# Performance work log

Measured on AMD Instinct MI355X. Metric: run time of the kernel, lower is better.

The kernel has to match this reference:

```python
import jax, jax.numpy as jnp
import numpy as np

EMBED_DIM = 1024
NUM_HEADS = 16
HEAD_DIM = EMBED_DIM // NUM_HEADS
SCALE = HEAD_DIM ** -0.5


def setup_inputs() -> dict:
    key = jax.random.key(0)
    ks = jax.random.split(key, 9)
    B, S, D = 32, 577, EMBED_DIM
    std = 1.0 / np.sqrt(D)
    inp = {
        "hidden_states": jax.random.normal(ks[0], (B, S, D), dtype=jnp.float32),
        "q_w": jax.random.normal(ks[1], (D, D), dtype=jnp.float32) * std,
        "q_b": jax.random.normal(ks[2], (D,), dtype=jnp.float32) * 0.01,
        "k_w": jax.random.normal(ks[3], (D, D), dtype=jnp.float32) * std,
        "k_b": jax.random.normal(ks[4], (D,), dtype=jnp.float32) * 0.01,
        "v_w": jax.random.normal(ks[5], (D, D), dtype=jnp.float32) * std,
        "v_b": jax.random.normal(ks[6], (D,), dtype=jnp.float32) * 0.01,
        "o_w": jax.random.normal(ks[7], (D, D), dtype=jnp.float32) * std,
        "o_b": jax.random.normal(ks[8], (D,), dtype=jnp.float32) * 0.01,
    }
    return inp


def reference(hidden_states, q_w, q_b, k_w, k_b, v_w, v_b, o_w, o_b):
    B, S, D = hidden_states.shape
    H, Dh = NUM_HEADS, HEAD_DIM

    def proj(w, b):
        # torch Linear: x @ w.T + b ; reshape to [B, H, S, Dh]
        y = jnp.einsum('bsd,ed->bse', hidden_states, w) + b
        return y.reshape(B, S, H, Dh).transpose(0, 2, 1, 3)

    q = proj(q_w, q_b)
    k = proj(k_w, k_b)
    v = proj(v_w, v_b)

    scores = jnp.einsum('bhqd,bhkd->bhqk', q * SCALE, k)  # [B,H,S,S]
    attn = jax.nn.softmax(scores, axis=-1)
    out = jnp.einsum('bhqk,bhkd->bhqd', attn, v)  # [B,H,S,Dh]
    out = out.transpose(0, 2, 1, 3).reshape(B, S, D)
    return jnp.einsum('bsd,ed->bse', out, o_w) + o_b
```

## Files before the change

### kernel.cpp

```cpp
#include <hip/hip_runtime.h>
#include <hip/hip_bf16.h>
#include <stdint.h>

#define B_   32
#define S_   577
#define SP   640
#define D_   1024
#define H_   16
#define DH   64
#define BH_  (B_*H_)
#define M_   (B_*S_)
#define MP2  18688
#define SCALE_ 0.125f
#define LOG2E_ 1.44269504088896f

typedef __bf16 bf16;
typedef __bf16 bf16x8 __attribute__((ext_vector_type(8)));
typedef __bf16 bf16x4 __attribute__((ext_vector_type(4)));
typedef float  f32x4  __attribute__((ext_vector_type(4)));

__device__ __forceinline__ void gload16(const bf16* g, bf16* l) {
    __builtin_amdgcn_global_load_lds((__attribute__((address_space(1))) void*)g,
                                     (__attribute__((address_space(3))) void*)l, 16, 0, 0);
}

__global__ void cast_kernel(const float* __restrict__ in, bf16* __restrict__ out, int n4) {
    int i = blockIdx.x * blockDim.x + threadIdx.x;
    if (i >= n4) return;
    float4 v = ((const float4*)in)[i];
    bf16x4 o;
    o[0] = (bf16)v.x; o[1] = (bf16)v.y; o[2] = (bf16)v.z; o[3] = (bf16)v.w;
    ((bf16x4*)out)[i] = o;
}

__global__ void cast4_kernel(const float* __restrict__ w0, const float* __restrict__ w1,
                             const float* __restrict__ w2, const float* __restrict__ w3,
                             bf16* __restrict__ o0, bf16* __restrict__ o1,
                             bf16* __restrict__ o2, bf16* __restrict__ o3) {
    int i = blockIdx.x * blockDim.x + threadIdx.x;
    int seg = i >> 18, r = i & 262143;
    const float* in = (seg == 0) ? w0 : (seg == 1) ? w1 : (seg == 2) ? w2 : w3;
    bf16* out       = (seg == 0) ? o0 : (seg == 1) ? o1 : (seg == 2) ? o2 : o3;
    float4 v = ((const float4*)in)[r];
    bf16x4 o;
    o[0] = (bf16)v.x; o[1] = (bf16)v.y; o[2] = (bf16)v.z; o[3] = (bf16)v.w;
    ((bf16x4*)out)[r] = o;
}

__device__ __forceinline__ void stage256(const bf16* __restrict__ A, const bf16* __restrict__ B,
                                         int m0, int n0, int K, int kt, bf16* SMbuf) {
    const int tid = threadIdx.x;
    const int wave = tid >> 6;
    #pragma unroll
    for (int ld = 0; ld < 8; ++ld) {
        int li  = ld * 512 + tid;
        int row = (li >> 3) & 255;
        int ch  = (li & 7) ^ (row & 7);
        const bf16* g = ((ld < 4) ? (A + (size_t)(m0 + row) * K)
                                  : (B + (size_t)(n0 + row) * K)) + kt * 64 + ch * 8;
        bf16* l = SMbuf + (size_t)(ld * 512 + wave * 64) * 8;
        gload16(g, l);
    }
}

__device__ __forceinline__ void compute256(const bf16* SMbuf, f32x4 acc[8][4],
                                           int wm, int wn, int r16, int c4) {
    #pragma unroll
    for (int kk = 0; kk < 2; ++kk) {
        bf16x8 bq[4];
        #pragma unroll
        for (int j = 0; j < 4; ++j) {
            int row = wn * 64 + j * 16 + r16;
            int c   = (kk * 4 + c4) ^ (row & 7);
            bq[j] = *(const bf16x8*)(SMbuf + 16384 + row * 64 + c * 8);
        }
        #pragma unroll
        for (int i = 0; i < 8; ++i) {
            int row = wm * 128 + i * 16 + r16;
            int c   = (kk * 4 + c4) ^ (row & 7);
            bf16x8 a = *(const bf16x8*)(SMbuf + row * 64 + c * 8);
            #pragma unroll
            for (int j = 0; j < 4; ++j)
                acc[i][j] = __builtin_amdgcn_mfma_f32_16x16x32_bf16(a, bq[j], acc[i][j], 0, 0, 0);
        }
    }
}

__global__ __launch_bounds__(512, 2) void gemm_qkv(const bf16* __restrict__ A, const bf16* __restrict__ Bw,
                                                   const float* __restrict__ qb, const float* __restrict__ kb,
                                                   const float* __restrict__ vb,
                                                   bf16* __restrict__ qk, bf16* __restrict__ vT) {
    __shared__ __align__(16) bf16 SM[2 * 32768];
    const int bx = blockIdx.x;
    const int bm = bx / 12, bn = bx % 12;
    const int m0 = bm * 256, n0 = bn * 256;
    const int tid = threadIdx.x;
    const int lane = tid & 63, wave = tid >> 6;
    const int wm = wave >> 2, wn = wave & 3;
    const int r16 = lane & 15, c4 = lane >> 4;

    f32x4 acc[8][4];
    #pragma unroll
    for (int i = 0; i < 8; ++i)
        #pragma unroll
        for (int j = 0; j < 4; ++j)
            #pragma unroll
            for (int r = 0; r < 4; ++r) acc[i][j][r] = 0.0f;

    stage256(A, Bw, m0, n0, 1024, 0, SM);
    __syncthreads();
    for (int kt = 0; kt < 16; ++kt) {
        if (kt < 15) stage256(A, Bw, m0, n0, 1024, kt + 1, SM + ((kt + 1) & 1) * 32768);
        compute256(SM + (kt & 1) * 32768, acc, wm, wn, r16, c4);
        __syncthreads();
    }

    if (bn < 8) {
        const float* barr = (bn < 4) ? qb : kb;
        const float mul = (bn < 4) ? SCALE_ * LOG2E_ : 1.0f;
        #pragma unroll
        for (int j = 0; j < 4; ++j) {
            int n = n0 + wn * 64 + j * 16 + r16;
            float bias = barr[n & 1023];
            #pragma unroll
            for (int i = 0; i < 8; ++i) {
                #pragma unroll
                for (int r = 0; r < 4; ++r) {
                    int m = m0 + wm * 128 + i * 16 + c4 * 4 + r;
                    if (m < M_) qk[(size_t)m * 2048 + n] = (bf16)((acc[i][j][r] + bias) * mul);
                }
            }
        }
    } else {
        const int bnp = bn - 8;
        bf16* Ts = SM;
        #pragma unroll
        for (int mh = 0; mh < 2; ++mh) {
            if (wm == mh) {
                #pragma unroll
                for (int j = 0; j < 4; ++j) {
                    int nl = wn * 64 + j * 16 + r16;
                    float bias = vb[bnp * 256 + nl];
                    #pragma unroll
                    for (int i = 0; i < 8; ++i) {
                        #pragma unroll
                        for (int r = 0; r < 4; ++r) {
                            int tr = i * 16 + c4 * 4 + r;
                            Ts[tr * 259 + nl] = (bf16)(acc[i][j][r] + bias);
                        }
                    }
                }
            }
            __syncthreads();
            {
                int ml = tid & 127, nh = tid >> 7;
                int gm = m0 + mh * 128 + ml;
                if (gm < M_) {
                    unsigned bb = (unsigned)gm / 577u, s = (unsigned)gm - bb * 577u;
                    bf16* dst = vT + ((size_t)((bb * 16 + bnp * 4 + nh) * 64)) * SP + s;
                    const bf16* src = Ts + ml * 259 + nh * 64;
                    #pragma unroll 8
                    for (int j = 0; j < 64; ++j) dst[(size_t)j * SP] = src[j];
                }
            }
            __syncthreads();
        }
    }
}

__device__ __forceinline__ void stage_out(const bf16* __restrict__ A, const bf16* __restrict__ B,
                                          int m0, int n0, int kt, bf16* SMbuf) {
    const int tid = threadIdx.x;
    const int wave = tid >> 6;
    #pragma unroll
    for (int ld = 0; ld < 2; ++ld) {
        int li  = ld * 512 + tid;
        int row = li >> 3;
        int ch  = (li & 7) ^ (row & 7);
        gload16(A + (size_t)(m0 + row) * 1024 + kt * 64 + ch * 8,
                SMbuf + (size_t)(ld * 512 + wave * 64) * 8);
    }
    #pragma unroll
    for (int ld = 0; ld < 4; ++ld) {
        int li  = ld * 512 + tid;
        int row = li >> 3;
        int ch  = (li & 7) ^ (row & 7);
        gload16(B + (size_t)(n0 + row) * 1024 + kt * 64 + ch * 8,
                SMbuf + 8192 + (size_t)(ld * 512 + wave * 64) * 8);
    }
}

__global__ __launch_bounds__(512, 2) void gemm_out(const bf16* __restrict__ A, const bf16* __restrict__ Bw,
                                                   const float* __restrict__ ob, float* __restrict__ out) {
    __shared__ __align__(16) bf16 SM[2 * 24576];
    const int bx = blockIdx.x;
    const int bm = bx >> 2, bn = bx & 3;
    const int m0 = bm * 128, n0 = bn * 256;
    const int tid = threadIdx.x;
    const int lane = tid & 63, wave = tid >> 6;
    const int wm = wave >> 2, wn = wave & 3;
    const int r16 = lane & 15, c4 = lane >> 4;

    f32x4 acc[4][4];
    #pragma unroll
    for (int i = 0; i < 4; ++i)
        #pragma unroll
        for (int j = 0; j < 4; ++j)
            #pragma unroll
            for (int r = 0; r < 4; ++r) acc[i][j][r] = 0.0f;

    stage_out(A, Bw, m0, n0, 0, SM);
    __syncthreads();
    for (int kt = 0; kt < 16; ++kt) {
        if (kt < 15) stage_out(A, Bw, m0, n0, kt + 1, SM + ((kt + 1) & 1) * 24576);
        const bf16* SMbuf = SM + (kt & 1) * 24576;
        #pragma unroll
        for (int kk = 0; kk < 2; ++kk) {
            bf16x8 bq[4];
            #pragma unroll
            for (int j = 0; j < 4; ++j) {
                int row = wn * 64 + j * 16 + r16;
                int c   = (kk * 4 + c4) ^ (row & 7);
                bq[j] = *(const bf16x8*)(SMbuf + 8192 + row * 64 + c * 8);
            }
            #pragma unroll
            for (int i = 0; i < 4; ++i) {
                int row = wm * 64 + i * 16 + r16;
                int c   = (kk * 4 + c4) ^ (row & 7);
                bf16x8 a = *(const bf16x8*)(SMbuf + row * 64 + c * 8);
                #pragma unroll
                for (int j = 0; j < 4; ++j)
                    acc[i][j] = __builtin_amdgcn_mfma_f32_16x16x32_bf16(a, bq[j], acc[i][j], 0, 0, 0);
            }
        }
        __syncthreads();
    }

    #pragma unroll
    for (int j = 0; j < 4; ++j) {
        int n = n0 + wn * 64 + j * 16 + r16;
        float bias = ob[n];
        #pragma unroll
        for (int i = 0; i < 4; ++i) {
            #pragma unroll
            for (int r = 0; r < 4; ++r) {
                int m = m0 + wm * 64 + i * 16 + c4 * 4 + r;
                if (m < M_) out[(size_t)m * 1024 + n] = acc[i][j][r] + bias;
            }
        }
    }
}

__global__ __launch_bounds__(256) void attn_kernel(const bf16* __restrict__ qk,
                                                   const bf16* __restrict__ vT, bf16* __restrict__ obuf) {
    __shared__ __align__(16) bf16 KV[2][2][4096];
    __shared__ __align__(16) char Pls[4 * 2048];
    const int orig = blockIdx.x;
    const int xcd = orig & 7;
    const int t   = orig >> 3;
    const int qt  = t % 5, bhg = t / 5;
    const int bh  = bhg * 8 + xcd;
    const int b   = bh >> 4, h = bh & 15;
    const int tid = threadIdx.x;
    const int lane = tid & 63, wave = tid >> 6;
    const int r16 = lane & 15, c4 = lane >> 4;
    const int q0  = qt * 128 + wave * 32;
    const int swz = (r16 & 7) << 4;

    const bf16* qp = qk + (size_t)(b * 577) * 2048 + h * 64;
    const bf16* kp = qp + 1024;
    const bf16* vp = vT + (size_t)bh * 64 * SP;

    bf16x8 aq[2][2];
    #pragma unroll
    for (int qf = 0; qf < 2; ++qf)
        #pragma unroll
        for (int c = 0; c < 2; ++c)
            aq[qf][c] = *(const bf16x8*)(qp + (size_t)(q0 + qf * 16 + r16) * 2048 + c * 32 + c4 * 8);

    float mi[2] = {-3.0e38f, -3.0e38f};
    float li[2] = {0.0f, 0.0f};
    f32x4 accO[2][4];
    #pragma unroll
    for (int qf = 0; qf < 2; ++qf)
        #pragma unroll
        for (int nt = 0; nt < 4; ++nt)
            #pragma unroll
            for (int r = 0; r < 4; ++r) accO[qf][nt][r] = 0.0f;

    char* pbase = Pls + wave * 2048 + r16 * 128;

    auto stageKV = [&](int kt, int buf) {
        #pragma unroll
        for (int half = 0; half < 2; ++half) {
            int li  = half * 256 + tid;
            int row = li >> 3;
            int ch  = (li & 7) ^ (row & 7);
            bf16* lk = &KV[buf][0][(size_t)(half * 256 + wave * 64) * 8];
            bf16* lv = &KV[buf][1][(size_t)(half * 256 + wave * 64) * 8];
            gload16(kp + (size_t)(kt * 64 + row) * 2048 + ch * 8, lk);
            gload16(vp + (size_t)row * SP + kt * 64 + ch * 8, lv);
        }
    };

    stageKV(0, 0);
    __syncthreads();

    for (int kt = 0; kt < 10; ++kt) {
        const int buf = kt & 1;
        if (kt < 9) stageKV(kt + 1, buf ^ 1);

        bf16x8 kf[4][2];
        #pragma unroll
        for (int nt = 0; nt < 4; ++nt)
            #pragma unroll
            for (int c = 0; c < 2; ++c) {
                int row = nt * 16 + r16;
                int cc  = (c * 4 + c4) ^ (row & 7);
                kf[nt][c] = *(const bf16x8*)(&KV[buf][0][row * 64 + cc * 8]);
            }
        f32x4 sc[2][4];
        #pragma unroll
        for (int qf = 0; qf < 2; ++qf)
            #pragma unroll
            for (int nt = 0; nt < 4; ++nt) {
                f32x4 z = {0.0f, 0.0f, 0.0f, 0.0f};
                z = __builtin_amdgcn_mfma_f32_16x16x32_bf16(kf[nt][0], aq[qf][0], z, 0, 0, 0);
                sc[qf][nt] = __builtin_amdgcn_mfma_f32_16x16x32_bf16(kf[nt][1], aq[qf][1], z, 0, 0, 0);
            }

        bf16x8 vf[4][2];
        #pragma unroll
        for (int ntd = 0; ntd < 4; ++ntd)
            #pragma unroll
            for (int kk = 0; kk < 2; ++kk) {
                int row = ntd * 16 + r16;
                int cc  = (kk * 4 + c4) ^ (row & 7);
                vf[ntd][kk] = *(const bf16x8*)(&KV[buf][1][row * 64 + cc * 8]);
            }

        #pragma unroll
        for (int qf = 0; qf < 2; ++qf) {
            if (kt == 9) {
                #pragma unroll
                for (int nt = 0; nt < 4; ++nt)
                    #pragma unroll
                    for (int r = 0; r < 4; ++r)
                        if (576 + nt * 16 + c4 * 4 + r >= S_) sc[qf][nt][r] = -3.0e38f;
            }
            float pmax = sc[qf][0][0];
            #pragma unroll
            for (int nt = 0; nt < 4; ++nt)
                #pragma unroll
                for (int r = 0; r < 4; ++r) pmax = fmaxf(pmax, sc[qf][nt][r]);
            pmax = fmaxf(pmax, __shfl_xor(pmax, 16));
            pmax = fmaxf(pmax, __shfl_xor(pmax, 32));

            const bool vrow = (q0 + qf * 16 + r16) < S_;
            int ok = (!vrow) || (pmax <= mi[qf] + 8.0f);
            if (!__all(ok)) {
                float mnew = fmaxf(mi[qf], pmax);
                float fsc  = __builtin_amdgcn_exp2f(mi[qf] - mnew);
                mi[qf] = mnew;
                li[qf] *= fsc;
                float fs0 = __shfl(fsc, c4 * 4 + 0);
                float fs1 = __shfl(fsc, c4 * 4 + 1);
                float fs2 = __shfl(fsc, c4 * 4 + 2);
                float fs3 = __shfl(fsc, c4 * 4 + 3);
                #pragma unroll
                for (int nt = 0; nt < 4; ++nt) {
                    accO[qf][nt][0] *= fs0; accO[qf][nt][1] *= fs1;
                    accO[qf][nt][2] *= fs2; accO[qf][nt][3] *= fs3;
                }
            }
            float p[4][4];
            float rs = 0.0f;
            #pragma unroll
            for (int nt = 0; nt < 4; ++nt)
                #pragma unroll
                for (int r = 0; r < 4; ++r) {
                    p[nt][r] = __builtin_amdgcn_exp2f(sc[qf][nt][r] - mi[qf]);
                    rs += p[nt][r];
                }
            rs += __shfl_xor(rs, 16);
            rs += __shfl_xor(rs, 32);
            li[qf] += rs;
            #pragma unroll
            for (int nt = 0; nt < 4; ++nt) {
                bf16x4 pk;
                pk[0] = (bf16)p[nt][0]; pk[1] = (bf16)p[nt][1];
                pk[2] = (bf16)p[nt][2]; pk[3] = (bf16)p[nt][3];
                *(bf16x4*)(pbase + ((nt * 32 + c4 * 8) ^ swz)) = pk;
            }

            bf16x8 pf[2];
            #pragma unroll
            for (int kk = 0; kk < 2; ++kk)
                pf[kk] = *(const bf16x8*)(pbase + ((kk * 64 + c4 * 16) ^ swz));
            #pragma unroll
            for (int ntd = 0; ntd < 4; ++ntd)
                #pragma unroll
                for (int kk = 0; kk < 2; ++kk)
                    accO[qf][ntd] = __builtin_amdgcn_mfma_f32_16x16x32_bf16(pf[kk], vf[ntd][kk], accO[qf][ntd], 0, 0, 0);
        }

        __syncthreads();
    }

    #pragma unroll
    for (int qf = 0; qf < 2; ++qf) {
        float inv = 1.0f / li[qf];
        float rl0 = __shfl(inv, c4 * 4 + 0);
        float rl1 = __shfl(inv, c4 * 4 + 1);
        float rl2 = __shfl(inv, c4 * 4 + 2);
        float rl3 = __shfl(inv, c4 * 4 + 3);
        #pragma unroll
        for (int ntd = 0; ntd < 4; ++ntd) {
            #pragma unroll
            for (int r = 0; r < 4; ++r) {
                int s = q0 + qf * 16 + c4 * 4 + r;
                if (s < S_) {
                    float rl = (r == 0) ? rl0 : (r == 1) ? rl1 : (r == 2) ? rl2 : rl3;
                    obuf[((size_t)(b * S_ + s)) * 1024 + h * 64 + ntd * 16 + r16] =
                        (bf16)(accO[qf][ntd][r] * rl);
                }
            }
        }
    }
}

extern "C" void kernel_launch(void* const* d_in, const int* in_sizes, int n_in,
                              void* d_out, int out_size, void* d_ws, size_t ws_size,
                              hipStream_t stream) {
    const float* hs = (const float*)d_in[0];
    const float* qw = (const float*)d_in[1];
    const float* qb = (const float*)d_in[2];
    const float* kw = (const float*)d_in[3];
    const float* kb = (const float*)d_in[4];
    const float* vw = (const float*)d_in[5];
    const float* vb = (const float*)d_in[6];
    const float* ow = (const float*)d_in[7];
    const float* ob = (const float*)d_in[8];

    char* ws = (char*)d_ws;
    size_t off = 0;
    auto alloc = [&](size_t bytes) { void* p = ws + off; off += (bytes + 255) & ~255UL; return p; };
    bf16* hsA  = (bf16*)alloc((size_t)MP2 * 1024 * 2);
    bf16* wqkv = (bf16*)alloc((size_t)3072 * 1024 * 2);
    bf16* wo   = (bf16*)alloc((size_t)1024 * 1024 * 2);
    bf16* qk   = (bf16*)alloc((size_t)MP2 * 2048 * 2);
    bf16* vT   = (bf16*)alloc((size_t)BH_ * 64 * SP * 2);

    hipMemsetAsync(vT, 0, (size_t)BH_ * 64 * SP * 2, stream);

    int n4h = M_ * 1024 / 4;
    cast_kernel<<<(n4h + 255) / 256, 256, 0, stream>>>(hs, hsA, n4h);
    cast4_kernel<<<4096, 256, 0, stream>>>(qw, kw, vw, ow,
                                           wqkv, wqkv + 1048576, wqkv + 2097152, wo);

    gemm_qkv<<<73 * 12, 512, 0, stream>>>(hsA, wqkv, qb, kb, vb, qk, vT);
    attn_kernel<<<2560, 256, 0, stream>>>(qk, vT, hsA);
    gemm_out<<<145 * 4, 512, 0, stream>>>(hsA, wo, ob, (float*)d_out);
}
```

Baseline: 369.2 us.

## Enlarge attention query tile, fuse cast kernels, zero only V padding

The attention kernel now gives each block 256 query rows (64 per wave, four 16-row fragments) across 3 query tiles instead of 128 rows across 5, so each K/V tile staged in LDS is reused by more queries. Fragments lying entirely past the sequence end are skipped. The two fp32-to-bf16 cast kernels are merged into one launch, and the full-buffer memset of vT is replaced by a small kernel that zeros only the padded tail columns. The larger query tile raises register pressure and can lower occupancy, and fewer blocks are launched, which may balance worse across CUs.

```diff
diff --git a/kernel.cpp b/kernel.cpp
--- a/kernel.cpp
+++ b/kernel.cpp
@@ -24,27 +24,33 @@
                                      (__attribute__((address_space(3))) void*)l, 16, 0, 0);
 }
 
-__global__ void cast_kernel(const float* __restrict__ in, bf16* __restrict__ out, int n4) {
+__global__ void cast_all(const float* __restrict__ hs, const float* __restrict__ qw,
+                         const float* __restrict__ kw, const float* __restrict__ vw,
+                         const float* __restrict__ ow,
+                         bf16* __restrict__ hsA, bf16* __restrict__ wq, bf16* __restrict__ wk,
+                         bf16* __restrict__ wv, bf16* __restrict__ wo) {
+    const int N4H = M_ * 256;
     int i = blockIdx.x * blockDim.x + threadIdx.x;
-    if (i >= n4) return;
-    float4 v = ((const float4*)in)[i];
-    bf16x4 o;
-    o[0] = (bf16)v.x; o[1] = (bf16)v.y; o[2] = (bf16)v.z; o[3] = (bf16)v.w;
-    ((bf16x4*)out)[i] = o;
-}
-
-__global__ void cast4_kernel(const float* __restrict__ w0, const float* __restrict__ w1,
-                             const float* __restrict__ w2, const float* __restrict__ w3,
-                             bf16* __restrict__ o0, bf16* __restrict__ o1,
-                             bf16* __restrict__ o2, bf16* __restrict__ o3) {
-    int i = blockIdx.x * blockDim.x + threadIdx.x;
-    int seg = i >> 18, r = i & 262143;
-    const float* in = (seg == 0) ? w0 : (seg == 1) ? w1 : (seg == 2) ? w2 : w3;
-    bf16* out       = (seg == 0) ? o0 : (seg == 1) ? o1 : (seg == 2) ? o2 : o3;
+    if (i >= N4H + 4 * 262144) return;
+    const float* in; bf16* out; int r;
+    if (i < N4H) { in = hs; out = hsA; r = i; }
+    else {
+        int j = i - N4H, seg = j >> 18; r = j & 262143;
+        in  = (seg == 0) ? qw : (seg == 1) ? kw : (seg == 2) ? vw : ow;
+        out = (seg == 0) ? wq : (seg == 1) ? wk : (seg == 2) ? wv : wo;
+    }
     float4 v = ((const float4*)in)[r];
     bf16x4 o;
     o[0] = (bf16)v.x; o[1] = (bf16)v.y; o[2] = (bf16)v.z; o[3] = (bf16)v.w;
     ((bf16x4*)out)[r] = o;
+}
+
+__global__ void zero_vpad(bf16* __restrict__ vT) {
+    int i = blockIdx.x * blockDim.x + threadIdx.x;
+    if (i >= BH_ * 64) return;
+    bf16* row = vT + (size_t)i * SP + S_;
+    #pragma unroll
+    for (int j = 0; j < SP - S_; ++j) row[j] = (bf16)0.0f;
 }
 
 __device__ __forceinline__ void stage256(const bf16* __restrict__ A, const bf16* __restrict__ B,
@@ -258,31 +264,31 @@
     const int orig = blockIdx.x;
     const int xcd = orig & 7;
     const int t   = orig >> 3;
-    const int qt  = t % 5, bhg = t / 5;
+    const int qt  = t % 3, bhg = t / 3;
     const int bh  = bhg * 8 + xcd;
     const int b   = bh >> 4, h = bh & 15;
     const int tid = threadIdx.x;
     const int lane = tid & 63, wave = tid >> 6;
     const int r16 = lane & 15, c4 = lane >> 4;
-    const int q0  = qt * 128 + wave * 32;
+    const int q0  = qt * 256 + wave * 64;
     const int swz = (r16 & 7) << 4;
 
     const bf16* qp = qk + (size_t)(b * 577) * 2048 + h * 64;
     const bf16* kp = qp + 1024;
     const bf16* vp = vT + (size_t)bh * 64 * SP;
 
-    bf16x8 aq[2][2];
-    #pragma unroll
-    for (int qf = 0; qf < 2; ++qf)
+    bf16x8 aq[4][2];
+    #pragma unroll
+    for (int qf = 0; qf < 4; ++qf)
         #pragma unroll
         for (int c = 0; c < 2; ++c)
             aq[qf][c] = *(const bf16x8*)(qp + (size_t)(q0 + qf * 16 + r16) * 2048 + c * 32 + c4 * 8);
 
-    float mi[2] = {-3.0e38f, -3.0e38f};
-    float li[2] = {0.0f, 0.0f};
-    f32x4 accO[2][4];
-    #pragma unroll
-    for (int qf = 0; qf < 2; ++qf)
+    float mi[4] = {-3.0e38f, -3.0e38f, -3.0e38f, -3.0e38f};
+    float li[4] = {0.0f, 0.0f, 0.0f, 0.0f};
+    f32x4 accO[4][4];
+    #pragma unroll
+    for (int qf = 0; qf < 4; ++qf)
         #pragma unroll
         for (int nt = 0; nt < 4; ++nt)
             #pragma unroll
@@ -319,16 +325,6 @@
                 int cc  = (c * 4 + c4) ^ (row & 7);
                 kf[nt][c] = *(const bf16x8*)(&KV[buf][0][row * 64 + cc * 8]);
             }
-        f32x4 sc[2][4];
-        #pragma unroll
-        for (int qf = 0; qf < 2; ++qf)
-            #pragma unroll
-            for (int nt = 0; nt < 4; ++nt) {
-                f32x4 z = {0.0f, 0.0f, 0.0f, 0.0f};
-                z = __builtin_amdgcn_mfma_f32_16x16x32_bf16(kf[nt][0], aq[qf][0], z, 0, 0, 0);
-                sc[qf][nt] = __builtin_amdgcn_mfma_f32_16x16x32_bf16(kf[nt][1], aq[qf][1], z, 0, 0, 0);
-            }
-
         bf16x8 vf[4][2];
         #pragma unroll
         for (int ntd = 0; ntd < 4; ++ntd)
@@ -340,75 +336,84 @@
             }
 
         #pragma unroll
-        for (int qf = 0; qf < 2; ++qf) {
-            if (kt == 9) {
+        for (int qf = 0; qf < 4; ++qf) {
+            if (q0 + qf * 16 < S_) {
+                f32x4 sc[4];
+                #pragma unroll
+                for (int nt = 0; nt < 4; ++nt) {
+                    f32x4 z = {0.0f, 0.0f, 0.0f, 0.0f};
+                    z = __builtin_amdgcn_mfma_f32_16x16x32_bf16(kf[nt][0], aq[qf][0], z, 0, 0, 0);
+                    sc[nt] = __builtin_amdgcn_mfma_f32_16x16x32_bf16(kf[nt][1], aq[qf][1], z, 0, 0, 0);
+                }
+                if (kt == 9) {
+                    #pragma unroll
+                    for (int nt = 0; nt < 4; ++nt)
+                        #pragma unroll
+                        for (int r = 0; r < 4; ++r)
+                            if (576 + nt * 16 + c4 * 4 + r >= S_) sc[nt][r] = -3.0e38f;
+                }
+                float pmax = sc[0][0];
                 #pragma unroll
                 for (int nt = 0; nt < 4; ++nt)
                     #pragma unroll
-                    for (int r = 0; r < 4; ++r)
-                        if (576 + nt * 16 + c4 * 4 + r >= S_) sc[qf][nt][r] = -3.0e38f;
-            }
-            float pmax = sc[qf][0][0];
-            #pragma unroll
-            for (int nt = 0; nt < 4; ++nt)
-                #pragma unroll
-                for (int r = 0; r < 4; ++r) pmax = fmaxf(pmax, sc[qf][nt][r]);
-            pmax = fmaxf(pmax, __shfl_xor(pmax, 16));
-            pmax = fmaxf(pmax, __shfl_xor(pmax, 32));
-
-            const bool vrow = (q0 + qf * 16 + r16) < S_;
-            int ok = (!vrow) || (pmax <= mi[qf] + 8.0f);
-            if (!__all(ok)) {
-                float mnew = fmaxf(mi[qf], pmax);
-                float fsc  = __builtin_amdgcn_exp2f(mi[qf] - mnew);
-                mi[qf] = mnew;
-                li[qf] *= fsc;
-                float fs0 = __shfl(fsc, c4 * 4 + 0);
-                float fs1 = __shfl(fsc, c4 * 4 + 1);
-                float fs2 = __shfl(fsc, c4 * 4 + 2);
-                float fs3 = __shfl(fsc, c4 * 4 + 3);
+                    for (int r = 0; r < 4; ++r) pmax = fmaxf(pmax, sc[nt][r]);
+                pmax = fmaxf(pmax, __shfl_xor(pmax, 16));
+                pmax = fmaxf(pmax, __shfl_xor(pmax, 32));
+
+                const bool vrow = (q0 + qf * 16 + r16) < S_;
+                int ok = (!vrow) || (pmax <= mi[qf] + 8.0f);
+                if (!__all(ok)) {
+                    float mnew = fmaxf(mi[qf], pmax);
+                    float fsc  = __builtin_amdgcn_exp2f(mi[qf] - mnew);
+                    mi[qf] = mnew;
+                    li[qf] *= fsc;
+                    float fs0 = __shfl(fsc, c4 * 4 + 0);
+                    float fs1 = __shfl(fsc, c4 * 4 + 1);
+                    float fs2 = __shfl(fsc, c4 * 4 + 2);
+                    float fs3 = __shfl(fsc, c4 * 4 + 3);
+                    #pragma unroll
+                    for (int nt = 0; nt < 4; ++nt) {
+                        accO[qf][nt][0] *= fs0; accO[qf][nt][1] *= fs1;
+                        accO[qf][nt][2] *= fs2; accO[qf][nt][3] *= fs3;
+                    }
+                }
+                float p[4][4];
+                float rs = 0.0f;
+                #pragma unroll
+                for (int nt = 0; nt < 4; ++nt)
+                    #pragma unroll
+                    for (int r = 0; r < 4; ++r) {
+                        p[nt][r] = __builtin_amdgcn_exp2f(sc[nt][r] - mi[qf]);
+                        rs += p[nt][r];
+                    }
+                rs += __shfl_xor(rs, 16);
+                rs += __shfl_xor(rs, 32);
+                li[qf] += rs;
                 #pragma unroll
                 for (int nt = 0; nt < 4; ++nt) {
-                    accO[qf][nt][0] *= fs0; accO[qf][nt][1] *= fs1;
-                    accO[qf][nt][2] *= fs2; accO[qf][nt][3] *= fs3;
-                }
-            }
-            float p[4][4];
-            float rs = 0.0f;
-            #pragma unroll
-            for (int nt = 0; nt < 4; ++nt)
-                #pragma unroll
-                for (int r = 0; r < 4; ++r) {
-                    p[nt][r] = __builtin_amdgcn_exp2f(sc[qf][nt][r] - mi[qf]);
-                    rs += p[nt][r];
-                }
-            rs += __shfl_xor(rs, 16);
-            rs += __shfl_xor(rs, 32);
-            li[qf] += rs;
-            #pragma unroll
-            for (int nt = 0; nt < 4; ++nt) {
-                bf16x4 pk;
-                pk[0] = (bf16)p[nt][0]; pk[1] = (bf16)p[nt][1];
-                pk[2] = (bf16)p[nt][2]; pk[3] = (bf16)p[nt][3];
-                *(bf16x4*)(pbase + ((nt * 32 + c4 * 8) ^ swz)) = pk;
-            }
-
-            bf16x8 pf[2];
-            #pragma unroll
-            for (int kk = 0; kk < 2; ++kk)
-                pf[kk] = *(const bf16x8*)(pbase + ((kk * 64 + c4 * 16) ^ swz));
-            #pragma unroll
-            for (int ntd = 0; ntd < 4; ++ntd)
+                    bf16x4 pk;
+                    pk[0] = (bf16)p[nt][0]; pk[1] = (bf16)p[nt][1];
+                    pk[2] = (bf16)p[nt][2]; pk[3] = (bf16)p[nt][3];
+                    *(bf16x4*)(pbase + ((nt * 32 + c4 * 8) ^ swz)) = pk;
+                }
+                bf16x8 pf[2];
                 #pragma unroll
                 for (int kk = 0; kk < 2; ++kk)
-                    accO[qf][ntd] = __builtin_amdgcn_mfma_f32_16x16x32_bf16(pf[kk], vf[ntd][kk], accO[qf][ntd], 0, 0, 0);
+                    pf[kk] = *(const bf16x8*)(pbase + ((kk * 64 + c4 * 16) ^ swz));
+                #pragma unroll
+                for (int ntd = 0; ntd < 4; ++ntd)
+                    #pragma unroll
+                    for (int kk = 0; kk < 2; ++kk)
+                        accO[qf][ntd] = __builtin_amdgcn_mfma_f32_16x16x32_bf16(pf[kk], vf[ntd][kk], accO[qf][ntd], 0, 0, 0);
+            }
         }
 
         __syncthreads();
     }
 
     #pragma unroll
-    for (int qf = 0; qf < 2; ++qf) {
+    for (int qf = 0; qf < 4; ++qf) {
+        if (q0 + qf * 16 >= S_) continue;
         float inv = 1.0f / li[qf];
         float rl0 = __shfl(inv, c4 * 4 + 0);
         float rl1 = __shfl(inv, c4 * 4 + 1);
@@ -451,14 +456,13 @@
     bf16* qk   = (bf16*)alloc((size_t)MP2 * 2048 * 2);
     bf16* vT   = (bf16*)alloc((size_t)BH_ * 64 * SP * 2);
 
-    hipMemsetAsync(vT, 0, (size_t)BH_ * 64 * SP * 2, stream);
-
-    int n4h = M_ * 1024 / 4;
-    cast_kernel<<<(n4h + 255) / 256, 256, 0, stream>>>(hs, hsA, n4h);
-    cast4_kernel<<<4096, 256, 0, stream>>>(qw, kw, vw, ow,
-                                           wqkv, wqkv + 1048576, wqkv + 2097152, wo);
+    zero_vpad<<<(BH_ * 64 + 255) / 256, 256, 0, stream>>>(vT);
+
+    int n4all = M_ * 256 + 4 * 262144;
+    cast_all<<<(n4all + 255) / 256, 256, 0, stream>>>(hs, qw, kw, vw, ow,
+                                                      hsA, wqkv, wqkv + 1048576, wqkv + 2097152, wo);
 
     gemm_qkv<<<73 * 12, 512, 0, stream>>>(hsA, wqkv, qb, kb, vb, qk, vT);
-    attn_kernel<<<2560, 256, 0, stream>>>(qk, vT, hsA);
+    attn_kernel<<<1536, 256, 0, stream>>>(qk, vT, hsA);
     gemm_out<<<145 * 4, 512, 0, stream>>>(hsA, wo, ob, (float*)d_out);
 }
```

New measurement: 436.0 us. +18.1%, slower.
